# Kernel optimization log

Measured on AMD Instinct MI355X. Metric: run time of the kernel, lower is better.

## Reference

```python
import jax, jax.numpy as jnp
import numpy as np

NUM_EMBEDDINGS = 16384
EMBEDDING_DIM = 512
COMMITMENT_COST = 0.25  # legacy: vq_loss = commit + beta * codebook
NORM_EPS = 1e-12  # F.normalize default eps


def setup_inputs() -> dict:
    key = jax.random.key(0)
    k_z, k_emb, k_w, k_b = jax.random.split(key, 4)
    z = jax.random.normal(k_z, (8, 1024, EMBEDDING_DIM), dtype=jnp.float32)
    # frozen codebook, init normal with std = D^{-0.5}
    embedding_weight = jax.random.normal(k_emb, (NUM_EMBEDDINGS, EMBEDDING_DIM), dtype=jnp.float32) * (EMBEDDING_DIM ** -0.5)
    # learnable projection (torch Linear: y = x @ W.T + b, W is [out, in])
    bound = 1.0 / np.sqrt(EMBEDDING_DIM)
    proj_w = jax.random.uniform(k_w, (EMBEDDING_DIM, EMBEDDING_DIM), dtype=jnp.float32, minval=-bound, maxval=bound)
    proj_b = jax.random.uniform(k_b, (EMBEDDING_DIM,), dtype=jnp.float32, minval=-bound, maxval=bound)
    scale = jnp.asarray(10.0, dtype=jnp.float32)
    return {"z": z, "embedding_weight": embedding_weight, "proj_w": proj_w, "proj_b": proj_b, "scale": scale}


def _l2_normalize(x):
    n = jnp.linalg.norm(x, axis=-1, keepdims=True)
    return x / jnp.maximum(n, NORM_EPS)


def reference(z, embedding_weight, proj_w, proj_b, scale):
    B, N, D = z.shape
    z_flat = z.reshape(-1, D)                                   # [M, D]
    quant_codebook = embedding_weight @ proj_w.T + proj_b       # [K, D]
    z_n = _l2_normalize(z_flat)
    c_n = _l2_normalize(quant_codebook)
    distances = -(z_n @ c_n.T) * scale                          # [M, K]
    encoding_indices = jnp.argmin(distances, axis=1)            # [M]
    quantized = quant_codebook[encoding_indices].reshape(z.shape)
    commitment_loss = jnp.mean((jax.lax.stop_gradient(quantized) - z) ** 2)
    codebook_loss = jnp.mean((quantized - jax.lax.stop_gradient(z)) ** 2)
    vq_loss = commitment_loss + COMMITMENT_COST * codebook_loss  # legacy=True
    quantized = z + jax.lax.stop_gradient(quantized - z)         # straight-through
    encoding_indices = encoding_indices.reshape(B, N)
    return quantized, vq_loss, encoding_indices
```

## Files before the change

### kernel.cpp

```cpp
#include <hip/hip_runtime.h>
#include <math.h>


typedef _Float16 f16;
typedef _Float16 f16x8 __attribute__((ext_vector_type(8)));
typedef _Float16 f16x4 __attribute__((ext_vector_type(4)));
typedef short s16x8 __attribute__((ext_vector_type(8)));
typedef float f32x4 __attribute__((ext_vector_type(4)));
typedef unsigned int u32;
typedef unsigned long long u64;
typedef unsigned short ushort_t;

#define INV2048 (1.0f/2048.0f)
#define MARGIN  0.010f

#define OFF_Q    0u
#define OFF_EHI  33554432u
#define OFF_ELO  50331648u
#define OFF_WHI  67108864u
#define OFF_WLO  67633152u
#define OFF_CB   68157440u
#define OFF_ZB   84934656u
#define OFF_RL   93323264u
#define OFF_PK   OFF_EHI

__device__ __forceinline__ void gload_lds16(const void* g, void* l) {
  __builtin_amdgcn_global_load_lds(
      (const __attribute__((address_space(1))) u32*)g,
      (__attribute__((address_space(3))) u32*)l, 16, 0, 0);
}

__device__ __forceinline__ void stage_tile(const void* __restrict__ src, int row0,
                                           int kt, char* lds, int tid) {
#pragma unroll
  for (int i = 0; i < 4; ++i) {
    int lin = i * 256 + tid;
    int row = lin >> 3;
    int slot = lin & 7;
    int k8 = slot ^ (row & 7);
    const char* g = (const char*)src + (((size_t)(row0 + row)) << 10)
                    + (size_t)(kt * 128 + k8 * 16);
    gload_lds16(g, lds + lin * 16);
  }
}

__device__ __forceinline__ u64 make_key(float v, int idx) {
  u32 b = __float_as_uint(v);
  u32 m = (u32)((int)b >> 31) | 0x80000000u;
  return ((u64)(b ^ m) << 32) | (u32)(0x7FFFFFFF - idx);
}
__device__ __forceinline__ float key_val(u64 k) {
  u32 o = (u32)(k >> 32);
  u32 m = (o & 0x80000000u) ? 0x80000000u : 0xFFFFFFFFu;
  return __uint_as_float(o ^ m);
}
__device__ __forceinline__ int key_idx(u64 k) {
  return 0x7FFFFFFF - (int)(u32)(k & 0xFFFFFFFFu);
}
__device__ __forceinline__ u64 umax64(u64 a, u64 b) { return a > b ? a : b; }

#define LDS_AHI 0
#define LDS_ALO 16384
#define LDS_BHI 32768
#define LDS_BLO 49152

__global__ __launch_bounds__(256, 2) void k_gemm_codebook(
    const f16* __restrict__ Ahi, const f16* __restrict__ Alo,
    const f16* __restrict__ Bhi, const f16* __restrict__ Blo,
    const float* __restrict__ bias, float* __restrict__ Q) {
  __shared__ __align__(16) char lds[65536];
  f32x4 hh[4][4], xx[4][4];
  const int tid = threadIdx.x;
  const int m0 = blockIdx.y * 128;
  const int n0 = blockIdx.x * 128;
  const int l = tid & 63;
  const int wid = tid >> 6;
  const int wr = (wid >> 1) * 64;
  const int wc = (wid & 1) * 64;
  const int r7 = (l & 15) & 7;

#pragma unroll
  for (int a = 0; a < 4; ++a)
#pragma unroll
    for (int b = 0; b < 4; ++b) {
      hh[a][b] = (f32x4){0.f, 0.f, 0.f, 0.f};
      xx[a][b] = (f32x4){0.f, 0.f, 0.f, 0.f};
    }

  for (int kt = 0; kt < 8; ++kt) {
    stage_tile(Ahi, m0, kt, lds + LDS_AHI, tid);
    stage_tile(Alo, m0, kt, lds + LDS_ALO, tid);
    stage_tile(Bhi, n0, kt, lds + LDS_BHI, tid);
    stage_tile(Blo, n0, kt, lds + LDS_BLO, tid);
    __syncthreads();
#pragma unroll
    for (int ks = 0; ks < 2; ++ks) {
      const int kg = ks * 4 + (l >> 4);
      const int s = (kg ^ r7) * 16;
      const char* pa = lds + (wr + (l & 15)) * 128 + s;
      const char* pb = lds + (wc + (l & 15)) * 128 + s;
      f16x8 ahi[4], alo[4];
#pragma unroll
      for (int mf = 0; mf < 4; ++mf) {
        ahi[mf] = *(const f16x8*)(pa + LDS_AHI + mf * 2048);
        alo[mf] = *(const f16x8*)(pa + LDS_ALO + mf * 2048);
      }
#pragma unroll
      for (int nf = 0; nf < 4; ++nf) {
        f16x8 bhi = *(const f16x8*)(pb + LDS_BHI + nf * 2048);
        f16x8 blo = *(const f16x8*)(pb + LDS_BLO + nf * 2048);
#pragma unroll
        for (int mf = 0; mf < 4; ++mf) {
          hh[mf][nf] = __builtin_amdgcn_mfma_f32_16x16x32_f16(ahi[mf], bhi, hh[mf][nf], 0, 0, 0);
          xx[mf][nf] = __builtin_amdgcn_mfma_f32_16x16x32_f16(ahi[mf], blo, xx[mf][nf], 0, 0, 0);
          xx[mf][nf] = __builtin_amdgcn_mfma_f32_16x16x32_f16(alo[mf], bhi, xx[mf][nf], 0, 0, 0);
        }
      }
    }
    __syncthreads();
  }

#pragma unroll
  for (int mf = 0; mf < 4; ++mf)
#pragma unroll
    for (int nf = 0; nf < 4; ++nf)
#pragma unroll
      for (int j = 0; j < 4; ++j) {
        int row = m0 + wr + mf * 16 + (l >> 4) * 4 + j;
        int col = n0 + wc + nf * 16 + (l & 15);
        Q[(size_t)row * 512 + col] = hh[mf][nf][j] + xx[mf][nf][j] * INV2048 + bias[col];
      }
}

__global__ __launch_bounds__(256, 4) void k_gemm_coarse(
    const ushort_t* __restrict__ CB, const ushort_t* __restrict__ ZB,
    u64* __restrict__ pk) {
  __shared__ __align__(16) char lds[32768];
  f32x4 acc[4][4];
  const int tid = threadIdx.x;
  const int cb0 = blockIdx.x * 128;
  const int zb0 = blockIdx.y * 128;
  const int l = tid & 63;
  const int wid = tid >> 6;
  const int wr = (wid >> 1);
  const int wc = (wid & 1);

  const int rA0 = tid >> 2, sA0 = tid & 3;
  const int rA1 = (tid + 256) >> 2, sA1 = tid & 3;
  const u32 ga0 = (u32)(rA0 * 1024 + ((sA0 ^ (rA0 & 3)) * 16));
  const u32 ga1 = (u32)(rA1 * 1024 + ((sA1 ^ (rA1 & 3)) * 16));
  const char* gA = (const char*)CB + ((size_t)cb0 << 10);
  const char* gB = (const char*)ZB + ((size_t)zb0 << 10);
  const u32 d0 = (u32)tid * 16;
  const u32 d1 = d0 + 4096;

#define STAGE32(KT, BUF)                                                       \
  {                                                                            \
    char* db_ = lds + (BUF) * 16384;                                           \
    const u32 ko_ = (u32)(KT) * 64;                                            \
    gload_lds16(gA + ga0 + ko_, db_ + d0);                                     \
    gload_lds16(gA + ga1 + ko_, db_ + d1);                                     \
    gload_lds16(gB + ga0 + ko_, db_ + 8192 + d0);                              \
    gload_lds16(gB + ga1 + ko_, db_ + 8192 + d1);                              \
  }

  const u32 sphys = (u32)((((l >> 4)) ^ ((l & 15) & 3)) * 16);
  const u32 aoff = (u32)((wr * 64 + (l & 15)) * 64) + sphys;
  const u32 boff = 8192u + (u32)((wc * 64 + (l & 15)) * 64) + sphys;

#pragma unroll
  for (int a = 0; a < 4; ++a)
#pragma unroll
    for (int b = 0; b < 4; ++b) acc[a][b] = (f32x4){0.f, 0.f, 0.f, 0.f};

#define COMPUTE32(BUF)                                                         \
  {                                                                            \
    const char* base_ = lds + (BUF) * 16384;                                   \
    s16x8 af[4];                                                               \
    _Pragma("unroll") for (int mf = 0; mf < 4; ++mf)                           \
      af[mf] = *(const s16x8*)(base_ + aoff + mf * 1024);                      \
    _Pragma("unroll") for (int nf = 0; nf < 4; ++nf) {                         \
      s16x8 bf = *(const s16x8*)(base_ + boff + nf * 1024);                    \
      _Pragma("unroll") for (int mf = 0; mf < 4; ++mf)                         \
        acc[mf][nf] = __builtin_amdgcn_mfma_f32_16x16x32_bf16(af[mf], bf, acc[mf][nf], 0, 0, 0); \
    }                                                                          \
  }

  STAGE32(0, 0)
  __syncthreads();
#pragma unroll 2
  for (int kt = 0; kt < 15; ++kt) {
    STAGE32(kt + 1, (kt & 1) ^ 1)
    COMPUTE32(kt & 1)
    __syncthreads();
  }
  COMPUTE32(1)
  __syncthreads();

  float* cmax = (float*)lds;
  u32* cnt = (u32*)(lds + 1024);
  u64* slots = (u64*)(lds + 2048);

  float cm[4];
#pragma unroll
  for (int nf = 0; nf < 4; ++nf) {
    float m = acc[0][nf][0];
#pragma unroll
    for (int mf = 0; mf < 4; ++mf)
#pragma unroll
      for (int j = 0; j < 4; ++j) m = fmaxf(m, acc[mf][nf][j]);
    m = fmaxf(m, __shfl_xor(m, 16, 64));
    m = fmaxf(m, __shfl_xor(m, 32, 64));
    cm[nf] = m;
  }
  if (tid < 128) cnt[tid] = 0;
  slots[tid] = 0;
  slots[tid + 256] = 0;
  if ((l >> 4) == 0) {
#pragma unroll
    for (int nf = 0; nf < 4; ++nf)
      cmax[(wc * 64 + nf * 16 + l) * 2 + wr] = cm[nf];
  }
  __syncthreads();

#pragma unroll
  for (int nf = 0; nf < 4; ++nf) {
    int col = wc * 64 + nf * 16 + (l & 15);
    float thresh = fmaxf(cmax[col * 2], cmax[col * 2 + 1]) - MARGIN;
#pragma unroll
    for (int mf = 0; mf < 4; ++mf)
#pragma unroll
      for (int j = 0; j < 4; ++j) {
        float v = acc[mf][nf][j];
        if (v >= thresh) {
          int code = cb0 + wr * 64 + mf * 16 + ((l >> 4) << 2) + j;
          u32 p = atomicAdd(&cnt[col], 1u);
          if (p < 4) slots[col * 4 + p] = make_key(v, code);
        }
      }
  }
  __syncthreads();

  if (tid < 128) {
    size_t base = (((size_t)(zb0 + tid)) * 128 + blockIdx.x) * 4;
#pragma unroll
    for (int s = 0; s < 4; ++s) pk[base + s] = slots[tid * 4 + s];
  }
#undef STAGE32
#undef COMPUTE32
}

__global__ __launch_bounds__(256) void k_split(const float* __restrict__ src,
                                               f16* __restrict__ hi,
                                               f16* __restrict__ lo, int n4) {
  int i = blockIdx.x * 256 + threadIdx.x;
  if (i >= n4) return;
  const float4 v = ((const float4*)src)[i];
  f16 h0 = (f16)v.x, h1 = (f16)v.y, h2 = (f16)v.z, h3 = (f16)v.w;
  ((f16x4*)hi)[i] = (f16x4){h0, h1, h2, h3};
  ((f16x4*)lo)[i] = (f16x4){(f16)((v.x - (float)h0) * 2048.0f),
                            (f16)((v.y - (float)h1) * 2048.0f),
                            (f16)((v.z - (float)h2) * 2048.0f),
                            (f16)((v.w - (float)h3) * 2048.0f)};
}

__device__ __forceinline__ ushort_t f2bf_rne(float f) {
  u32 b = __float_as_uint(f);
  b += 0x7FFFu + ((b >> 16) & 1u);
  return (ushort_t)(b >> 16);
}

__global__ __launch_bounds__(256) void k_norm_bf16(const float* __restrict__ src,
                                                   ushort_t* __restrict__ dst) {
  __shared__ float red[256];
  const int row = blockIdx.x, t = threadIdx.x;
  float q0 = src[(size_t)row * 512 + t];
  float q1 = src[(size_t)row * 512 + t + 256];
  red[t] = q0 * q0 + q1 * q1;
  __syncthreads();
  for (int s = 128; s > 0; s >>= 1) {
    if (t < s) red[t] += red[t + s];
    __syncthreads();
  }
  float inv = 1.0f / fmaxf(sqrtf(red[0]), 1e-12f);
  dst[(size_t)row * 512 + t] = f2bf_rne(q0 * inv);
  dst[(size_t)row * 512 + t + 256] = f2bf_rne(q1 * inv);
}

__global__ __launch_bounds__(256) void k_rescore_gather(
    const u64* __restrict__ pk, const float* __restrict__ Q,
    const float* __restrict__ z, float* __restrict__ outq,
    float* __restrict__ outidx, float* __restrict__ rloss) {
  __shared__ float sz[512];
  __shared__ double redd[8];
  __shared__ u64 redk[4];
  __shared__ int cand[64];
  __shared__ int ccount;
  const int row = blockIdx.x, t = threadIdx.x;

  sz[t] = z[(size_t)row * 512 + t];
  sz[t + 256] = z[(size_t)row * 512 + t + 256];
  if (t == 0) ccount = 0;

  u64 k1 = pk[(size_t)row * 512 + t * 2];
  u64 k2 = pk[(size_t)row * 512 + t * 2 + 1];
  u64 km = umax64(k1, k2);
  for (int m = 1; m < 64; m <<= 1)
    km = umax64(km, (u64)__shfl_xor((long long)km, m));
  if ((t & 63) == 0) redk[t >> 6] = km;
  __syncthreads();
  u64 gk = umax64(umax64(redk[0], redk[1]), umax64(redk[2], redk[3]));
  float thresh = key_val(gk) - MARGIN;

  if (key_val(k1) >= thresh) { int p = atomicAdd(&ccount, 1); if (p < 64) cand[p] = key_idx(k1); }
  if (key_val(k2) >= thresh) { int p = atomicAdd(&ccount, 1); if (p < 64) cand[p] = key_idx(k2); }
  __syncthreads();
  int nc = ccount < 64 ? ccount : 64;

  double bs = -1e300;
  int bi = 0x7FFFFFFF;
  for (int c = 0; c < nc; ++c) {
    int code = cand[c];
    const float* Qr = Q + (size_t)code * 512;
    double dotp = 0.0, qq = 0.0;
#pragma unroll
    for (int h = 0; h < 2; ++h) {
      int d = t + h * 256;
      double qv = (double)Qr[d];
      dotp += (double)sz[d] * qv;
      qq += qv * qv;
    }
    for (int m = 1; m < 64; m <<= 1) {
      dotp += __shfl_xor(dotp, m);
      qq += __shfl_xor(qq, m);
    }
    if ((t & 63) == 0) { redd[t >> 6] = dotp; redd[4 + (t >> 6)] = qq; }
    __syncthreads();
    double dsum = redd[0] + redd[1] + redd[2] + redd[3];
    double qsum = redd[4] + redd[5] + redd[6] + redd[7];
    double s = dsum / fmax(sqrt(qsum), 1e-12);
    if (s > bs || (s == bs && code < bi)) { bs = s; bi = code; }
    __syncthreads();
  }

  const float* Qb = Q + (size_t)bi * 512;
  double lsum = 0.0;
#pragma unroll
  for (int h = 0; h < 2; ++h) {
    int d = t + h * 256;
    float qv = Qb[d], zv = sz[d];
    outq[(size_t)row * 512 + d] = zv + (qv - zv);
    float df = qv - zv;
    lsum += (double)df * (double)df;
  }
  for (int m = 1; m < 64; m <<= 1) lsum += __shfl_xor(lsum, m);
  if ((t & 63) == 0) redd[t >> 6] = lsum;
  __syncthreads();
  if (t == 0) {
    rloss[row] = (float)(redd[0] + redd[1] + redd[2] + redd[3]);
    outidx[row] = (float)bi;
  }
}

__global__ __launch_bounds__(256) void k_loss_final(const float* __restrict__ rloss,
                                                    float* __restrict__ out_loss) {
  __shared__ float sl[256];
  int t = threadIdx.x;
  float s = 0.f;
#pragma unroll
  for (int i = 0; i < 32; ++i) s += rloss[t + i * 256];
  sl[t] = s;
  __syncthreads();
  for (int k = 128; k > 0; k >>= 1) {
    if (t < k) sl[t] += sl[t + k];
    __syncthreads();
  }
  if (t == 0) out_loss[0] = 1.25f * sl[0] / 4194304.0f;
}

extern "C" void kernel_launch(void* const* d_in, const int* in_sizes, int n_in,
                              void* d_out, int out_size, void* d_ws, size_t ws_size,
                              hipStream_t stream) {
  const float* z = (const float*)d_in[0];
  const float* emb = (const float*)d_in[1];
  const float* pw = (const float*)d_in[2];
  const float* pb = (const float*)d_in[3];

  char* ws = (char*)d_ws;
  float* Q = (float*)(ws + OFF_Q);
  f16* ehi = (f16*)(ws + OFF_EHI);
  f16* elo = (f16*)(ws + OFF_ELO);
  f16* whi = (f16*)(ws + OFF_WHI);
  f16* wlo = (f16*)(ws + OFF_WLO);
  ushort_t* cb = (ushort_t*)(ws + OFF_CB);
  ushort_t* zb = (ushort_t*)(ws + OFF_ZB);
  u64* pk = (u64*)(ws + OFF_PK);
  float* rloss = (float*)(ws + OFF_RL);

  float* outq = (float*)d_out;
  float* outloss = outq + 4194304;
  float* outidx = outq + 4194305;

  k_split<<<8192, 256, 0, stream>>>(emb, ehi, elo, 2097152);
  k_split<<<256, 256, 0, stream>>>(pw, whi, wlo, 65536);
  k_norm_bf16<<<8192, 256, 0, stream>>>(z, zb);
  k_gemm_codebook<<<dim3(4, 128), 256, 0, stream>>>(ehi, elo, whi, wlo, pb, Q);
  k_norm_bf16<<<16384, 256, 0, stream>>>(Q, cb);
  k_gemm_coarse<<<dim3(128, 64), 256, 0, stream>>>(cb, zb, pk);
  k_rescore_gather<<<8192, 256, 0, stream>>>(pk, Q, z, outq, outidx, rloss);
  k_loss_final<<<1, 256, 0, stream>>>(rloss, outloss);
}
```

Measured before the change: 307.6 us.

## Fuse codebook normalization into GEMM epilogue and merge preprocessing kernels

Removes the separate codebook L2-normalize kernel. The projection GEMM epilogue now writes the unnormalized bf16 codebook and accumulates per-row squared norms with atomics, and the coarse GEMM scales its scores by the inverse norm before the max/threshold step. The two split kernels and the z normalize kernel are merged into one launch. The LDS swizzle pattern in the coarse GEMM also changes. This saves a full pass over the 16384x512 codebook and several launches, at the cost of a memset, float atomics, and bf16 rounding applied before normalization rather than after.

```diff
diff --git a/kernel.cpp b/kernel.cpp
--- a/kernel.cpp
+++ b/kernel.cpp
@@ -19,9 +19,10 @@
 #define OFF_ELO  50331648u
 #define OFF_WHI  67108864u
 #define OFF_WLO  67633152u
-#define OFF_CB   68157440u
+#define OFF_QB   68157440u
 #define OFF_ZB   84934656u
 #define OFF_RL   93323264u
+#define OFF_NORM 93356032u
 #define OFF_PK   OFF_EHI
 
 __device__ __forceinline__ void gload_lds16(const void* g, void* l) {
@@ -59,6 +60,47 @@
 }
 __device__ __forceinline__ u64 umax64(u64 a, u64 b) { return a > b ? a : b; }
 
+__device__ __forceinline__ ushort_t f2bf_rne(float f) {
+  u32 b = __float_as_uint(f);
+  b += 0x7FFFu + ((b >> 16) & 1u);
+  return (ushort_t)(b >> 16);
+}
+
+__global__ __launch_bounds__(256) void k_pre(
+    const float* __restrict__ emb, const float* __restrict__ pw,
+    const float* __restrict__ z, f16* __restrict__ ehi, f16* __restrict__ elo,
+    f16* __restrict__ whi, f16* __restrict__ wlo, ushort_t* __restrict__ zb) {
+  __shared__ float red[256];
+  const int bid = blockIdx.x, t = threadIdx.x;
+  if (bid < 8448) {
+    const float* src;
+    f16 *hi, *lo;
+    int i;
+    if (bid < 8192) { src = emb; hi = ehi; lo = elo; i = bid * 256 + t; }
+    else            { src = pw;  hi = whi; lo = wlo; i = (bid - 8192) * 256 + t; }
+    const float4 v = ((const float4*)src)[i];
+    f16 h0 = (f16)v.x, h1 = (f16)v.y, h2 = (f16)v.z, h3 = (f16)v.w;
+    ((f16x4*)hi)[i] = (f16x4){h0, h1, h2, h3};
+    ((f16x4*)lo)[i] = (f16x4){(f16)((v.x - (float)h0) * 2048.0f),
+                              (f16)((v.y - (float)h1) * 2048.0f),
+                              (f16)((v.z - (float)h2) * 2048.0f),
+                              (f16)((v.w - (float)h3) * 2048.0f)};
+  } else {
+    const int row = bid - 8448;
+    float q0 = z[(size_t)row * 512 + t];
+    float q1 = z[(size_t)row * 512 + t + 256];
+    red[t] = q0 * q0 + q1 * q1;
+    __syncthreads();
+    for (int s = 128; s > 0; s >>= 1) {
+      if (t < s) red[t] += red[t + s];
+      __syncthreads();
+    }
+    float inv = 1.0f / fmaxf(sqrtf(red[0]), 1e-12f);
+    zb[(size_t)row * 512 + t] = f2bf_rne(q0 * inv);
+    zb[(size_t)row * 512 + t + 256] = f2bf_rne(q1 * inv);
+  }
+}
+
 #define LDS_AHI 0
 #define LDS_ALO 16384
 #define LDS_BHI 32768
@@ -67,7 +109,8 @@
 __global__ __launch_bounds__(256, 2) void k_gemm_codebook(
     const f16* __restrict__ Ahi, const f16* __restrict__ Alo,
     const f16* __restrict__ Bhi, const f16* __restrict__ Blo,
-    const float* __restrict__ bias, float* __restrict__ Q) {
+    const float* __restrict__ bias, float* __restrict__ Q,
+    ushort_t* __restrict__ Qb, float* __restrict__ norms) {
   __shared__ __align__(16) char lds[65536];
   f32x4 hh[4][4], xx[4][4];
   const int tid = threadIdx.x;
@@ -123,18 +166,26 @@
 #pragma unroll
   for (int mf = 0; mf < 4; ++mf)
 #pragma unroll
-    for (int nf = 0; nf < 4; ++nf)
-#pragma unroll
-      for (int j = 0; j < 4; ++j) {
-        int row = m0 + wr + mf * 16 + (l >> 4) * 4 + j;
+    for (int j = 0; j < 4; ++j) {
+      const int row = m0 + wr + mf * 16 + (l >> 4) * 4 + j;
+      float ss = 0.f;
+#pragma unroll
+      for (int nf = 0; nf < 4; ++nf) {
         int col = n0 + wc + nf * 16 + (l & 15);
-        Q[(size_t)row * 512 + col] = hh[mf][nf][j] + xx[mf][nf][j] * INV2048 + bias[col];
+        float q = hh[mf][nf][j] + xx[mf][nf][j] * INV2048 + bias[col];
+        Q[(size_t)row * 512 + col] = q;
+        Qb[(size_t)row * 512 + col] = f2bf_rne(q);
+        ss += q * q;
       }
+#pragma unroll
+      for (int m = 1; m < 16; m <<= 1) ss += __shfl_xor(ss, m, 64);
+      if ((l & 15) == 0) atomicAdd(&norms[row], ss);
+    }
 }
 
 __global__ __launch_bounds__(256, 4) void k_gemm_coarse(
     const ushort_t* __restrict__ CB, const ushort_t* __restrict__ ZB,
-    u64* __restrict__ pk) {
+    const float* __restrict__ norms, u64* __restrict__ pk) {
   __shared__ __align__(16) char lds[32768];
   f32x4 acc[4][4];
   const int tid = threadIdx.x;
@@ -146,9 +197,9 @@
   const int wc = (wid & 1);
 
   const int rA0 = tid >> 2, sA0 = tid & 3;
-  const int rA1 = (tid + 256) >> 2, sA1 = tid & 3;
-  const u32 ga0 = (u32)(rA0 * 1024 + ((sA0 ^ (rA0 & 3)) * 16));
-  const u32 ga1 = (u32)(rA1 * 1024 + ((sA1 ^ (rA1 & 3)) * 16));
+  const int rA1 = rA0 + 64;
+  const u32 ga0 = (u32)(rA0 * 1024 + ((sA0 ^ ((rA0 >> 1) & 3)) * 16));
+  const u32 ga1 = (u32)(rA1 * 1024 + ((sA0 ^ ((rA1 >> 1) & 3)) * 16));
   const char* gA = (const char*)CB + ((size_t)cb0 << 10);
   const char* gB = (const char*)ZB + ((size_t)zb0 << 10);
   const u32 d0 = (u32)tid * 16;
@@ -164,7 +215,7 @@
     gload_lds16(gB + ga1 + ko_, db_ + 8192 + d1);                              \
   }
 
-  const u32 sphys = (u32)((((l >> 4)) ^ ((l & 15) & 3)) * 16);
+  const u32 sphys = (u32)((((l >> 4)) ^ (((l & 15) >> 1) & 3)) * 16);
   const u32 aoff = (u32)((wr * 64 + (l & 15)) * 64) + sphys;
   const u32 boff = 8192u + (u32)((wc * 64 + (l & 15)) * 64) + sphys;
 
@@ -197,6 +248,15 @@
   COMPUTE32(1)
   __syncthreads();
 
+  float rs[16];
+#pragma unroll
+  for (int mf = 0; mf < 4; ++mf)
+#pragma unroll
+    for (int j = 0; j < 4; ++j) {
+      int code = cb0 + wr * 64 + mf * 16 + ((l >> 4) << 2) + j;
+      rs[mf * 4 + j] = 1.0f / fmaxf(sqrtf(norms[code]), 1e-12f);
+    }
+
   float* cmax = (float*)lds;
   u32* cnt = (u32*)(lds + 1024);
   u64* slots = (u64*)(lds + 2048);
@@ -204,11 +264,11 @@
   float cm[4];
 #pragma unroll
   for (int nf = 0; nf < 4; ++nf) {
-    float m = acc[0][nf][0];
+    float m = -INFINITY;
 #pragma unroll
     for (int mf = 0; mf < 4; ++mf)
 #pragma unroll
-      for (int j = 0; j < 4; ++j) m = fmaxf(m, acc[mf][nf][j]);
+      for (int j = 0; j < 4; ++j) m = fmaxf(m, acc[mf][nf][j] * rs[mf * 4 + j]);
     m = fmaxf(m, __shfl_xor(m, 16, 64));
     m = fmaxf(m, __shfl_xor(m, 32, 64));
     cm[nf] = m;
@@ -231,7 +291,7 @@
     for (int mf = 0; mf < 4; ++mf)
 #pragma unroll
       for (int j = 0; j < 4; ++j) {
-        float v = acc[mf][nf][j];
+        float v = acc[mf][nf][j] * rs[mf * 4 + j];
         if (v >= thresh) {
           int code = cb0 + wr * 64 + mf * 16 + ((l >> 4) << 2) + j;
           u32 p = atomicAdd(&cnt[col], 1u);
@@ -248,43 +308,6 @@
   }
 #undef STAGE32
 #undef COMPUTE32
-}
-
-__global__ __launch_bounds__(256) void k_split(const float* __restrict__ src,
-                                               f16* __restrict__ hi,
-                                               f16* __restrict__ lo, int n4) {
-  int i = blockIdx.x * 256 + threadIdx.x;
-  if (i >= n4) return;
-  const float4 v = ((const float4*)src)[i];
-  f16 h0 = (f16)v.x, h1 = (f16)v.y, h2 = (f16)v.z, h3 = (f16)v.w;
-  ((f16x4*)hi)[i] = (f16x4){h0, h1, h2, h3};
-  ((f16x4*)lo)[i] = (f16x4){(f16)((v.x - (float)h0) * 2048.0f),
-                            (f16)((v.y - (float)h1) * 2048.0f),
-                            (f16)((v.z - (float)h2) * 2048.0f),
-                            (f16)((v.w - (float)h3) * 2048.0f)};
-}
-
-__device__ __forceinline__ ushort_t f2bf_rne(float f) {
-  u32 b = __float_as_uint(f);
-  b += 0x7FFFu + ((b >> 16) & 1u);
-  return (ushort_t)(b >> 16);
-}
-
-__global__ __launch_bounds__(256) void k_norm_bf16(const float* __restrict__ src,
-                                                   ushort_t* __restrict__ dst) {
-  __shared__ float red[256];
-  const int row = blockIdx.x, t = threadIdx.x;
-  float q0 = src[(size_t)row * 512 + t];
-  float q1 = src[(size_t)row * 512 + t + 256];
-  red[t] = q0 * q0 + q1 * q1;
-  __syncthreads();
-  for (int s = 128; s > 0; s >>= 1) {
-    if (t < s) red[t] += red[t + s];
-    __syncthreads();
-  }
-  float inv = 1.0f / fmaxf(sqrtf(red[0]), 1e-12f);
-  dst[(size_t)row * 512 + t] = f2bf_rne(q0 * inv);
-  dst[(size_t)row * 512 + t + 256] = f2bf_rne(q1 * inv);
 }
 
 __global__ __launch_bounds__(256) void k_rescore_gather(
@@ -392,21 +415,20 @@
   f16* elo = (f16*)(ws + OFF_ELO);
   f16* whi = (f16*)(ws + OFF_WHI);
   f16* wlo = (f16*)(ws + OFF_WLO);
-  ushort_t* cb = (ushort_t*)(ws + OFF_CB);
+  ushort_t* qb = (ushort_t*)(ws + OFF_QB);
   ushort_t* zb = (ushort_t*)(ws + OFF_ZB);
   u64* pk = (u64*)(ws + OFF_PK);
   float* rloss = (float*)(ws + OFF_RL);
+  float* norms = (float*)(ws + OFF_NORM);
 
   float* outq = (float*)d_out;
   float* outloss = outq + 4194304;
   float* outidx = outq + 4194305;
 
-  k_split<<<8192, 256, 0, stream>>>(emb, ehi, elo, 2097152);
-  k_split<<<256, 256, 0, stream>>>(pw, whi, wlo, 65536);
-  k_norm_bf16<<<8192, 256, 0, stream>>>(z, zb);
-  k_gemm_codebook<<<dim3(4, 128), 256, 0, stream>>>(ehi, elo, whi, wlo, pb, Q);
-  k_norm_bf16<<<16384, 256, 0, stream>>>(Q, cb);
-  k_gemm_coarse<<<dim3(128, 64), 256, 0, stream>>>(cb, zb, pk);
+  hipMemsetAsync(norms, 0, 16384 * sizeof(float), stream);
+  k_pre<<<16640, 256, 0, stream>>>(emb, pw, z, ehi, elo, whi, wlo, zb);
+  k_gemm_codebook<<<dim3(4, 128), 256, 0, stream>>>(ehi, elo, whi, wlo, pb, Q, qb, norms);
+  k_gemm_coarse<<<dim3(128, 64), 256, 0, stream>>>(qb, zb, norms, pk);
   k_rescore_gather<<<8192, 256, 0, stream>>>(pk, Q, z, outq, outidx, rloss);
   k_loss_final<<<1, 256, 0, stream>>>(rloss, outloss);
 }
```

New measurement: 323.4 us. 1.05x slower.
